# Optimization experiments

Measured on AMD Instinct MI355X. Metric: run time of the kernel, lower is better.

The kernel has to match this reference:

```python
import jax, jax.numpy as jnp
import numpy as np

NUM_HEADS = 16
HEAD_DIM = 64
LN_EPS = 1e-12


def _interleave_pairs(a, b):
    # stack([a, b], -1).reshape(..., 2*d) -> interleaved on last dim
    return jnp.stack([a, b], axis=-1).reshape(a.shape[:-1] + (a.shape[-1] * 2,))


def _rotate_half(x):
    # stack([-x[..., 1::2], x[..., ::2]], -1).reshape_as(x)
    return _interleave_pairs(-x[..., 1::2], x[..., ::2])


def setup_inputs() -> dict:
    key = jax.random.key(0)
    ks = jax.random.split(key, 4)
    B, S, H = 4, 2048, 1024
    hidden_states = jax.random.normal(ks[0], (B, S, H), dtype=jnp.float32)
    sinusoidal_pos = jax.random.uniform(ks[1], (1, 1, S, HEAD_DIM), dtype=jnp.float32)
    ln_weight = jnp.ones((H,), dtype=jnp.float32)
    ln_bias = jnp.zeros((H,), dtype=jnp.float32)
    w_qkv = jax.random.normal(ks[2], (H, 3 * H), dtype=jnp.float32) * (1.0 / np.sqrt(H))
    b_qkv = jax.random.normal(ks[3], (3 * H,), dtype=jnp.float32) * 0.02
    return {"hidden_states": hidden_states, "sinusoidal_pos": sinusoidal_pos,
            "ln_weight": ln_weight, "ln_bias": ln_bias, "w_qkv": w_qkv, "b_qkv": b_qkv}


def reference(hidden_states, sinusoidal_pos, ln_weight, ln_bias, w_qkv, b_qkv):
    B, S, H = hidden_states.shape
    # LayerNorm
    mu = jnp.mean(hidden_states, axis=-1, keepdims=True)
    var = jnp.mean(jnp.square(hidden_states - mu), axis=-1, keepdims=True)
    h = (hidden_states - mu) * jax.lax.rsqrt(var + LN_EPS) * ln_weight + ln_bias
    # Fused QKV projection
    qkv = h @ w_qkv + b_qkv                       # [B, S, 3H]
    q, k, v = jnp.split(qkv, 3, axis=-1)
    def to_heads(x):
        return x.reshape(B, S, NUM_HEADS, HEAD_DIM).transpose(0, 2, 1, 3)  # [B, Hn, S, D]
    q, k, v = to_heads(q), to_heads(k), to_heads(v)
    # RoPE (RoFormer interleaved style)
    sin, cos = jnp.split(sinusoidal_pos, 2, axis=-1)      # each [1,1,S,D/2]
    sin_pos = _interleave_pairs(sin, sin)                 # [1,1,S,D]
    cos_pos = _interleave_pairs(cos, cos)
    q = q * cos_pos + _rotate_half(q) * sin_pos
    k = k * cos_pos + _rotate_half(k) * sin_pos
    # SDPA (non-causal, no mask, eval-mode dropout=0)
    scale = 1.0 / np.sqrt(HEAD_DIM)
    scores = jnp.einsum('bhqd,bhkd->bhqk', q, k) * scale
    probs = jax.nn.softmax(scores, axis=-1)
    ctx = jnp.einsum('bhqk,bhkd->bhqd', probs, v)         # [B, Hn, S, D]
    ctx = ctx.transpose(0, 2, 1, 3).reshape(B, S, H)
    return ctx
```

## Files before the change

kernel.cpp:

```cpp
#include <hip/hip_runtime.h>
#include <hip/hip_bf16.h>
#include <cstdint>
#include <cstddef>

#define DEVINL __device__ __forceinline__

typedef float f32x2 __attribute__((ext_vector_type(2)));
typedef float f32x4 __attribute__((ext_vector_type(4)));
typedef float f32x16 __attribute__((ext_vector_type(16)));
typedef short s16x8 __attribute__((ext_vector_type(8)));
typedef short s16x4 __attribute__((ext_vector_type(4)));

static constexpr int Sd = 2048;
static constexpr int Hd = 1024;
static constexpr int NHd = 16;
static constexpr int Dd = 64;
static constexpr int N3 = 3072;

DEVINL float bf2f(short u){
  unsigned int t = ((unsigned int)(unsigned short)u) << 16;
  float f; __builtin_memcpy(&f, &t, 4); return f;
}
DEVINL short f2bf(float f){
  unsigned int t; __builtin_memcpy(&t, &f, 4);
  unsigned int r = t + 0x7FFFu + ((t >> 16) & 1u);
  return (short)(r >> 16);
}

DEVINL void gld16(const short* g, short* l){
  __builtin_amdgcn_global_load_lds((const __attribute__((address_space(1))) unsigned int*)g,
                                   (__attribute__((address_space(3))) unsigned int*)l, 16, 0, 0);
}

DEVINL int cvtpk(float lo, float hi){
  int r; asm("v_cvt_pk_bf16_f32 %0, %1, %2" : "=v"(r) : "v"(lo), "v"(hi)); return r;
}

DEVINL float fexp2(float x){
#if __has_builtin(__builtin_amdgcn_exp2f)
  return __builtin_amdgcn_exp2f(x);
#else
  return exp2f(x);
#endif
}

DEVINL f32x16 z16(){
  f32x16 v;
  #pragma unroll
  for (int i=0;i<16;i++) v[i]=0.f;
  return v;
}

__global__ __launch_bounds__(256) void prep_kernel(const float* __restrict__ x,
                                                   const float* __restrict__ lw,
                                                   const float* __restrict__ lb,
                                                   short* __restrict__ h,
                                                   const float* __restrict__ w,
                                                   short* __restrict__ wT){
  int bid = blockIdx.x, tid = threadIdx.x;
  if (bid < 8192){
    const float* xr = x + (size_t)bid * Hd;
    f32x4 v = *(const f32x4*)(xr + tid*4);
    float s1 = v[0]+v[1]+v[2]+v[3];
    float s2 = v[0]*v[0]+v[1]*v[1]+v[2]*v[2]+v[3]*v[3];
    #pragma unroll
    for (int off = 1; off < 64; off <<= 1){ s1 += __shfl_xor(s1, off); s2 += __shfl_xor(s2, off); }
    __shared__ float red[8];
    if ((tid & 63) == 0){ red[(tid>>6)*2] = s1; red[(tid>>6)*2+1] = s2; }
    __syncthreads();
    s1 = red[0]+red[2]+red[4]+red[6];
    s2 = red[1]+red[3]+red[5]+red[7];
    float mu = s1 * (1.0f/Hd);
    float rstd = rsqrtf(s2*(1.0f/Hd) - mu*mu + 1e-12f);
    f32x4 wv = *(const f32x4*)(lw + tid*4);
    f32x4 bv = *(const f32x4*)(lb + tid*4);
    s16x4 o;
    #pragma unroll
    for (int i=0;i<4;i++) o[i] = f2bf((v[i]-mu)*rstd*wv[i] + bv[i]);
    *(s16x4*)(h + (size_t)bid*Hd + tid*4) = o;
  } else {
    __shared__ float t[32][33];
    int cid = bid - 8192;
    int n0 = (cid % 96)*32, k0 = (cid / 96)*32;
    int tx = tid & 31, ty = tid >> 5;
    #pragma unroll
    for (int i=0;i<4;i++) t[ty + i*8][tx] = w[(size_t)(k0 + ty + i*8)*N3 + n0 + tx];
    __syncthreads();
    #pragma unroll
    for (int i=0;i<4;i++) wT[(size_t)(n0 + ty + i*8)*Hd + k0 + tx] = f2bf(t[tx][ty + i*8]);
  }
}

__global__ __launch_bounds__(256) void gemm_kernel(const short* __restrict__ A,
                                                   const short* __restrict__ Bt,
                                                   const float* __restrict__ bias,
                                                   const float* __restrict__ sp,
                                                   short* __restrict__ qo,
                                                   short* __restrict__ ko,
                                                   short* __restrict__ vo){
  __shared__ alignas(16) char smem[49152];
  float* sps2 = (float*)smem;
  int bid = blockIdx.x;
  int xcd = bid & 7, idx = bid >> 3;
  int mt = xcd*8 + (idx & 7), nt = idx >> 3;
  int m0 = mt*128, n0 = nt*128;
  int tid = threadIdx.x, lane = tid & 63, wv = tid >> 6;
  int l15 = lane & 15, lq = lane >> 4;
  int wr = wv >> 1, wc = wv & 1;
  f32x4 zero = {0.f,0.f,0.f,0.f};
  f32x4 acc[4][4];
  #pragma unroll
  for (int m=0;m<4;m++)
    #pragma unroll
    for (int n=0;n<4;n++) acc[m][n] = zero;
  int rA = tid >> 2;
  int gA = (tid & 3) ^ ((rA >> 1) & 3);
  const short* gaA0 = A  + (size_t)(m0 + rA)*Hd + gA*8;
  const short* gaA1 = gaA0 + (size_t)64*Hd;
  const short* gaB0 = Bt + (size_t)(n0 + rA)*Hd + gA*8;
  const short* gaB1 = gaB0 + (size_t)64*Hd;
  int rsw2 = (l15 >> 1) & 3;
  int fcol = (lq ^ rsw2) * 8;
  int arow = (wr*64 + l15)*32 + fcol;
  int brow = (wc*64 + l15)*32 + fcol;

#define GSTAGE(bq_, t_) do { \
    short* dA = (short*)(smem + (bq_)*16384) + wv*512; \
    short* dB = (short*)(smem + (bq_)*16384 + 8192) + wv*512; \
    gld16(gaA0 + (t_)*32, dA); \
    gld16(gaA1 + (t_)*32, dA + 2048); \
    gld16(gaB0 + (t_)*32, dB); \
    gld16(gaB1 + (t_)*32, dB + 2048); \
  } while(0)

#define KBODY(bq_) do { \
    const short* Ab = (const short*)(smem + (bq_)*16384); \
    const short* Bb = (const short*)(smem + (bq_)*16384 + 8192); \
    s16x8 af[4], bf[4]; \
    _Pragma("unroll") \
    for (int m=0;m<4;m++) af[m] = *(const s16x8*)(Ab + arow + m*512); \
    _Pragma("unroll") \
    for (int n=0;n<4;n++) bf[n] = *(const s16x8*)(Bb + brow + n*512); \
    __builtin_amdgcn_s_setprio(1); \
    _Pragma("unroll") \
    for (int m=0;m<4;m++) \
      _Pragma("unroll") \
      for (int n=0;n<4;n++) \
        acc[m][n] = __builtin_amdgcn_mfma_f32_16x16x32_bf16(af[m], bf[n], acc[m][n], 0, 0, 0); \
    __builtin_amdgcn_s_setprio(0); \
  } while(0)

  GSTAGE(0, 0);
  GSTAGE(1, 1);
  int bq = 0;
  for (int t = 0; t < 31; ++t){
    asm volatile("s_waitcnt vmcnt(4)" ::: "memory");
    __builtin_amdgcn_s_barrier();
    __builtin_amdgcn_sched_barrier(0);
    if (t < 30){
      int bn = bq + 2; if (bn >= 3) bn -= 3;
      GSTAGE(bn, t+2);
    }
    KBODY(bq);
    ++bq; if (bq >= 3) bq = 0;
  }
  asm volatile("s_waitcnt vmcnt(0)" ::: "memory");
  __builtin_amdgcn_s_barrier();
  __builtin_amdgcn_sched_barrier(0);
  KBODY(bq);
#undef GSTAGE
#undef KBODY
  int part = nt >> 3;
  if (part == 2){
    #pragma unroll
    for (int n=0;n<4;n++){
      int c = n0 + wc*64 + n*16 + l15;
      float bv = bias[c];
      int hh = (c >> 6) & 15, d = c & 63;
      #pragma unroll
      for (int m=0;m<4;m++){
        int r0 = m0 + wr*64 + m*16 + lq*4;
        int b = r0 >> 11, s0r = r0 & 2047;
        s16x4 o;
        #pragma unroll
        for (int j=0;j<4;j++) o[j] = f2bf(acc[m][n][j] + bv);
        *(s16x4*)(vo + (((size_t)((b*NHd + hh)*Dd + d)) << 11) + s0r) = o;
      }
    }
  } else {
    __syncthreads();
    const float* gsp = sp + (size_t)(m0 & 2047)*64;
    #pragma unroll
    for (int u4=0; u4<4; ++u4){
      int u = tid + u4*256;
      int sl = u >> 3, dh4 = u & 7;
      f32x4 s4v = *(const f32x4*)(gsp + sl*64 + dh4*4);
      f32x4 c4v = *(const f32x4*)(gsp + sl*64 + 32 + dh4*4);
      float* w8 = sps2 + sl*66 + dh4*8;
      f32x2 p0 = {s4v[0], c4v[0]}, p1 = {s4v[1], c4v[1]};
      f32x2 p2 = {s4v[2], c4v[2]}, p3 = {s4v[3], c4v[3]};
      *(f32x2*)(w8)     = p0; *(f32x2*)(w8 + 2) = p1;
      *(f32x2*)(w8 + 4) = p2; *(f32x2*)(w8 + 6) = p3;
    }
    __syncthreads();
    short* dst = part == 0 ? qo : ko;
    float postscale = part == 0 ? 0.18033688011112042f : 1.0f;
    float sgnmul = (l15 & 1) ? 1.0f : -1.0f;
    float bvv[4]; int hhv[4], dv[4];
    #pragma unroll
    for (int n=0;n<4;n++){
      int c = n0 + wc*64 + n*16 + l15;
      bvv[n] = bias[c]; hhv[n] = (c >> 6) & 15; dv[n] = c & 63;
    }
    int dh0 = l15 >> 1;
    #pragma unroll
    for (int m=0;m<4;m++){
      #pragma unroll
      for (int j=0;j<4;j++){
        int sl = wr*64 + m*16 + lq*4 + j;
        const float* sb = sps2 + sl*66 + dh0*2;
        int r = m0 + sl;
        int b = r >> 11, s = r & 2047;
        #pragma unroll
        for (int n=0;n<4;n++){
          f32x2 sc = *(const f32x2*)(sb + n*16);
          float x = acc[m][n][j] + bvv[n];
          float xp = __shfl_xor(x, 1);
          float y = (x*sc[1] + sgnmul*xp*sc[0]) * postscale;
          dst[(((size_t)((b*NHd + hhv[n])*Sd + s)) << 6) + dv[n]] = f2bf(y);
        }
      }
    }
  }
}

__global__ __launch_bounds__(512, 4) void attn_kernel(const short* __restrict__ q,
                                                      const short* __restrict__ k,
                                                      const short* __restrict__ vT,
                                                      float* __restrict__ out){
  __shared__ alignas(16) short kbuf[2][8192];
  __shared__ alignas(16) short vbuf[2][8192];
  int bid = blockIdx.x;
  int xcd = bid & 7, w = bid >> 3;
  int bh = xcd*8 + (w >> 3), qb = w & 7;
  int tid = threadIdx.x, lane = tid & 63, wv = tid >> 6;
  int l31 = lane & 31, hi = lane >> 5;
  const short* kp = k  + ((size_t)bh << 17);
  const short* vp = vT + ((size_t)bh << 17);
  int qrow = qb*256 + wv*32 + l31;
  const short* qp = q + ((size_t)bh << 17) + (size_t)qrow*64;
  s16x8 qf[4];
  #pragma unroll
  for (int kk=0;kk<4;kk++) qf[kk] = *(const s16x8*)(qp + kk*16 + hi*8);
  int kc0 = tid,      kr0 = kc0 >> 3;
  int kc1 = tid+512,  kr1 = kc1 >> 3;
  int koff0 = kr0*64 + ((kc0 ^ kr0) & 7)*8;
  int koff1 = kr1*64 + ((kc1 ^ kr1) & 7)*8;
  int vr0 = tid >> 4,       vcc0 = tid & 15;
  int vr1 = (tid+512) >> 4, vcc1 = (tid+512) & 15;
  int voff0 = vr0*2048 + ((vcc0 & 8) | ((vcc0 ^ vr0) & 7))*8;
  int voff1 = vr1*2048 + ((vcc1 & 8) | ((vcc1 ^ vr1) & 7))*8;

  f32x16 ot0 = z16(), ot1 = z16();
  float m = -1e30f, lr = 0.f;
  int rsw = (l31 & 7);

#define STAGE(nb, t) do { \
    gld16(kp + (size_t)(t)*8192 + koff0, &kbuf[nb][0]    + wv*512); \
    gld16(kp + (size_t)(t)*8192 + koff1, &kbuf[nb][4096] + wv*512); \
    gld16(vp + (size_t)(t)*128  + voff0, &vbuf[nb][0]    + wv*512); \
    gld16(vp + (size_t)(t)*128  + voff1, &vbuf[nb][4096] + wv*512); \
  } while(0)

  STAGE(0, 0);
  __syncthreads();

  for (int t = 0; t < 16; ++t){
    int cur = t & 1;
    if (t < 15) STAGE(cur^1, t+1);
    #pragma unroll
    for (int h = 0; h < 2; ++h){
      const short* kb = &kbuf[cur][h*4096];
      const short* vb = &vbuf[cur][h*64];
      f32x16 s0 = z16(), s1 = z16();
      __builtin_amdgcn_s_setprio(1);
      #pragma unroll
      for (int kk=0;kk<4;kk++){
        s16x8 kf0 = *(const s16x8*)(kb + l31*64       + (((kk*2 + hi) ^ rsw)*8));
        s0 = __builtin_amdgcn_mfma_f32_32x32x16_bf16(kf0, qf[kk], s0, 0, 0, 0);
        s16x8 kf1 = *(const s16x8*)(kb + (32+l31)*64  + (((kk*2 + hi) ^ rsw)*8));
        s1 = __builtin_amdgcn_mfma_f32_32x32x16_bf16(kf1, qf[kk], s1, 0, 0, 0);
      }
      __builtin_amdgcn_s_setprio(0);
      float tm[16];
      #pragma unroll
      for (int i=0;i<16;i++) tm[i] = fmaxf(s0[i], s1[i]);
      #pragma unroll
      for (int off=8; off>=1; off>>=1)
        #pragma unroll
        for (int i=0;i<off;i++) tm[i] = fmaxf(tm[i], tm[i+off]);
      float pmax = fmaxf(tm[0], __shfl_xor(tm[0], 32));
      if (!__all(pmax - m <= 8.0f)){
        float mn = fmaxf(m, pmax);
        float al = fexp2(m - mn);
        m = mn; lr *= al;
        #pragma unroll
        for (int i=0;i<16;i++){ ot0[i] *= al; ot1[i] *= al; }
      }
      #pragma unroll
      for (int i=0;i<16;i++){ s0[i] = fexp2(s0[i]-m); s1[i] = fexp2(s1[i]-m); }
      float ra[16];
      #pragma unroll
      for (int i=0;i<16;i++) ra[i] = s0[i] + s1[i];
      #pragma unroll
      for (int off=8; off>=1; off>>=1)
        #pragma unroll
        for (int i=0;i<off;i++) ra[i] += ra[i+off];
      lr += ra[0];
      #pragma unroll
      for (int s4=0;s4<4;s4++){
        int base = (s4 & 1) * 8;
        int pkA0, pkA1, pkB0, pkB1;
        if (s4 < 2){
          pkA0 = cvtpk(s0[base],   s0[base+1]); pkA1 = cvtpk(s0[base+2], s0[base+3]);
          pkB0 = cvtpk(s0[base+4], s0[base+5]); pkB1 = cvtpk(s0[base+6], s0[base+7]);
        } else {
          pkA0 = cvtpk(s1[base],   s1[base+1]); pkA1 = cvtpk(s1[base+2], s1[base+3]);
          pkB0 = cvtpk(s1[base+4], s1[base+5]); pkB1 = cvtpk(s1[base+6], s1[base+7]);
        }
        int r0 = __shfl_xor(hi ? pkA0 : pkB0, 32);
        int r1 = __shfl_xor(hi ? pkA1 : pkB1, 32);
        union { int wq[4]; s16x8 v8; } u;
        u.wq[0] = hi ? r0   : pkA0;
        u.wq[1] = hi ? r1   : pkA1;
        u.wq[2] = hi ? pkB0 : r0;
        u.wq[3] = hi ? pkB1 : r1;
        __builtin_amdgcn_s_setprio(1);
        s16x8 vf0 = *(const s16x8*)(vb + l31*128      + (((s4*2 + hi) ^ rsw)*8));
        ot0 = __builtin_amdgcn_mfma_f32_32x32x16_bf16(vf0, u.v8, ot0, 0, 0, 0);
        s16x8 vf1 = *(const s16x8*)(vb + (32+l31)*128 + (((s4*2 + hi) ^ rsw)*8));
        ot1 = __builtin_amdgcn_mfma_f32_32x32x16_bf16(vf1, u.v8, ot1, 0, 0, 0);
        __builtin_amdgcn_s_setprio(0);
      }
    }
    __syncthreads();
  }
#undef STAGE
  float lrt = lr + __shfl_xor(lr, 32);
  float inv = 1.0f / lrt;
  int b = bh >> 4, hh = bh & 15;
  float* orow = out + ((size_t)(b*Sd + qrow) << 10) + hh*64;
  #pragma unroll
  for (int g=0; g<4; ++g){
    f32x4 w0, w1;
    #pragma unroll
    for (int j=0;j<4;j++){ w0[j] = ot0[4*g+j]*inv; w1[j] = ot1[4*g+j]*inv; }
    *(f32x4*)(orow + g*8 + 4*hi)      = w0;
    *(f32x4*)(orow + 32 + g*8 + 4*hi) = w1;
  }
}

extern "C" void kernel_launch(void* const* d_in, const int* in_sizes, int n_in,
                              void* d_out, int out_size, void* d_ws, size_t ws_size,
                              hipStream_t stream){
  const float* hs = (const float*)d_in[0];
  const float* sp = (const float*)d_in[1];
  const float* lw = (const float*)d_in[2];
  const float* lb = (const float*)d_in[3];
  const float* wq = (const float*)d_in[4];
  const float* bq = (const float*)d_in[5];
  float* out = (float*)d_out;
  char* ws = (char*)d_ws;
  short* h   = (short*)(ws);
  short* wT  = (short*)(ws + 16777216);
  short* qb_ = (short*)(ws + 23068672);
  short* kb_ = (short*)(ws + 23068672 + 16777216);
  short* vTb = (short*)(ws + 23068672 + 33554432);

  hipLaunchKernelGGL(prep_kernel,  dim3(11264),   dim3(256),   0, stream, hs, lw, lb, h, wq, wT);
  hipLaunchKernelGGL(gemm_kernel,  dim3(1536),    dim3(256),   0, stream, h, wT, bq, sp, qb_, kb_, vTb);
  hipLaunchKernelGGL(attn_kernel,  dim3(512),     dim3(512),   0, stream, qb_, kb_, vTb, out);
}
```

Baseline: 173.6 us.

## Enlarge QKV GEMM tile to 256x128 with BK=64 and 512 threads

The QKV projection GEMM moves from 128x128 tiles with 4 waves and a K step of 32 to 256x128 tiles with 8 waves and a K step of 64. It keeps the 3-stage LDS ring, now 48KB per stage, and uses an 8-way XOR swizzle. This halves the grid to 768 blocks and doubles the reuse of each B tile, cutting global/L2 traffic and per-K-step barrier overhead. In exchange, the 144KB LDS footprint limits each CU to one block, which reduces latency hiding across blocks.

New measurement: 172.6 us, median of 2. About the same (-0.6%).

```diff
diff --git a/kernel.cpp b/kernel.cpp
--- a/kernel.cpp
+++ b/kernel.cpp
@@ -91,19 +91,19 @@
   }
 }
 
-__global__ __launch_bounds__(256) void gemm_kernel(const short* __restrict__ A,
-                                                   const short* __restrict__ Bt,
-                                                   const float* __restrict__ bias,
-                                                   const float* __restrict__ sp,
-                                                   short* __restrict__ qo,
-                                                   short* __restrict__ ko,
-                                                   short* __restrict__ vo){
-  __shared__ alignas(16) char smem[49152];
+__global__ __launch_bounds__(512, 2) void gemm_kernel(const short* __restrict__ A,
+                                                      const short* __restrict__ Bt,
+                                                      const float* __restrict__ bias,
+                                                      const float* __restrict__ sp,
+                                                      short* __restrict__ qo,
+                                                      short* __restrict__ ko,
+                                                      short* __restrict__ vo){
+  __shared__ alignas(16) char smem[147456];
   float* sps2 = (float*)smem;
   int bid = blockIdx.x;
   int xcd = bid & 7, idx = bid >> 3;
-  int mt = xcd*8 + (idx & 7), nt = idx >> 3;
-  int m0 = mt*128, n0 = nt*128;
+  int mt = xcd*4 + (idx & 3), nt = idx >> 2;
+  int m0 = mt*256, n0 = nt*128;
   int tid = threadIdx.x, lane = tid & 63, wv = tid >> 6;
   int l15 = lane & 15, lq = lane >> 4;
   int wr = wv >> 1, wc = wv & 1;
@@ -113,51 +113,57 @@
   for (int m=0;m<4;m++)
     #pragma unroll
     for (int n=0;n<4;n++) acc[m][n] = zero;
-  int rA = tid >> 2;
-  int gA = (tid & 3) ^ ((rA >> 1) & 3);
-  const short* gaA0 = A  + (size_t)(m0 + rA)*Hd + gA*8;
-  const short* gaA1 = gaA0 + (size_t)64*Hd;
-  const short* gaB0 = Bt + (size_t)(n0 + rA)*Hd + gA*8;
-  const short* gaB1 = gaB0 + (size_t)64*Hd;
-  int rsw2 = (l15 >> 1) & 3;
-  int fcol = (lq ^ rsw2) * 8;
-  int arow = (wr*64 + l15)*32 + fcol;
-  int brow = (wc*64 + l15)*32 + fcol;
-
-#define GSTAGE(bq_, t_) do { \
-    short* dA = (short*)(smem + (bq_)*16384) + wv*512; \
-    short* dB = (short*)(smem + (bq_)*16384 + 8192) + wv*512; \
-    gld16(gaA0 + (t_)*32, dA); \
-    gld16(gaA1 + (t_)*32, dA + 2048); \
-    gld16(gaB0 + (t_)*32, dB); \
-    gld16(gaB1 + (t_)*32, dB + 2048); \
+  const short* srcA[4]; const short* srcB[2];
+  #pragma unroll
+  for (int i=0;i<4;i++){
+    int c = tid + i*512, r = c >> 3, g = (c & 7) ^ (r & 7);
+    srcA[i] = A + (size_t)(m0 + r)*Hd + g*8;
+  }
+  #pragma unroll
+  for (int i=0;i<2;i++){
+    int c = tid + i*512, r = c >> 3, g = (c & 7) ^ (r & 7);
+    srcB[i] = Bt + (size_t)(n0 + r)*Hd + g*8;
+  }
+  int rsw = l15 & 7;
+
+#define GSTAGE(q_, t_) do { \
+    short* bA = (short*)(smem + (q_)*49152); \
+    short* bB = bA + 16384; \
+    _Pragma("unroll") \
+    for (int i=0;i<4;i++) gld16(srcA[i] + (t_)*64, bA + wv*512 + i*4096); \
+    _Pragma("unroll") \
+    for (int i=0;i<2;i++) gld16(srcB[i] + (t_)*64, bB + wv*512 + i*4096); \
   } while(0)
 
-#define KBODY(bq_) do { \
-    const short* Ab = (const short*)(smem + (bq_)*16384); \
-    const short* Bb = (const short*)(smem + (bq_)*16384 + 8192); \
-    s16x8 af[4], bf[4]; \
+#define KBODY(q_) do { \
+    const short* bA = (const short*)(smem + (q_)*49152); \
+    const short* bB = bA + 16384; \
     _Pragma("unroll") \
-    for (int m=0;m<4;m++) af[m] = *(const s16x8*)(Ab + arow + m*512); \
-    _Pragma("unroll") \
-    for (int n=0;n<4;n++) bf[n] = *(const s16x8*)(Bb + brow + n*512); \
-    __builtin_amdgcn_s_setprio(1); \
-    _Pragma("unroll") \
-    for (int m=0;m<4;m++) \
+    for (int kh=0;kh<2;kh++){ \
+      s16x8 bf[4]; \
       _Pragma("unroll") \
       for (int n=0;n<4;n++) \
-        acc[m][n] = __builtin_amdgcn_mfma_f32_16x16x32_bf16(af[m], bf[n], acc[m][n], 0, 0, 0); \
-    __builtin_amdgcn_s_setprio(0); \
+        bf[n] = *(const s16x8*)(bB + (wc*64 + n*16 + l15)*64 + (((kh*4+lq)^rsw)*8)); \
+      __builtin_amdgcn_s_setprio(1); \
+      _Pragma("unroll") \
+      for (int m=0;m<4;m++){ \
+        s16x8 af = *(const s16x8*)(bA + (wr*64 + m*16 + l15)*64 + (((kh*4+lq)^rsw)*8)); \
+        _Pragma("unroll") \
+        for (int n=0;n<4;n++) \
+          acc[m][n] = __builtin_amdgcn_mfma_f32_16x16x32_bf16(af, bf[n], acc[m][n], 0, 0, 0); \
+      } \
+      __builtin_amdgcn_s_setprio(0); \
+    } \
   } while(0)
 
   GSTAGE(0, 0);
   GSTAGE(1, 1);
   int bq = 0;
-  for (int t = 0; t < 31; ++t){
-    asm volatile("s_waitcnt vmcnt(4)" ::: "memory");
+  for (int t = 0; t < 15; ++t){
+    asm volatile("s_waitcnt vmcnt(6)" ::: "memory");
     __builtin_amdgcn_s_barrier();
     __builtin_amdgcn_sched_barrier(0);
-    if (t < 30){
+    if (t < 14){
       int bn = bq + 2; if (bn >= 3) bn -= 3;
       GSTAGE(bn, t+2);
     }
@@ -192,7 +198,7 @@
     const float* gsp = sp + (size_t)(m0 & 2047)*64;
     #pragma unroll
     for (int u4=0; u4<4; ++u4){
-      int u = tid + u4*256;
+      int u = tid + u4*512;
       int sl = u >> 3, dh4 = u & 7;
       f32x4 s4v = *(const f32x4*)(gsp + sl*64 + dh4*4);
       f32x4 c4v = *(const f32x4*)(gsp + sl*64 + 32 + dh4*4);
@@ -378,6 +384,6 @@
   short* vTb = (short*)(ws + 23068672 + 33554432);
 
   hipLaunchKernelGGL(prep_kernel,  dim3(11264),   dim3(256),   0, stream, hs, lw, lb, h, wq, wT);
-  hipLaunchKernelGGL(gemm_kernel,  dim3(1536),    dim3(256),   0, stream, h, wT, bq, sp, qb_, kb_, vTb);
+  hipLaunchKernelGGL(gemm_kernel,  dim3(768),     dim3(512),   0, stream, h, wT, bq, sp, qb_, kb_, vTb);
   hipLaunchKernelGGL(attn_kernel,  dim3(512),     dim3(512),   0, stream, qb_, kb_, vTb, out);
 }
```
